# Kernel optimization log

Hardware: AMD Instinct MI355X
Metric: run time of the kernel (lower is better)

Reference implementation:

```python
import jax, jax.numpy as jnp
import numpy as np

K = 20
IN_CH = 128
OUT_CH = 128


def setup_inputs() -> dict:
    key = jax.random.key(0)
    k1, k2, k3, k4, k5, k6 = jax.random.split(key, 6)
    B, N = 2, 8192
    pos = jax.random.normal(k1, (B, N, 3), dtype=jnp.float32)
    features = jax.random.normal(k2, (B, N, IN_CH), dtype=jnp.float32)
    # fc = Linear(2C -> OUT) , ReLU, Linear(OUT -> OUT); stored as [in, out]
    s1 = 1.0 / np.sqrt(2 * IN_CH)
    s2 = 1.0 / np.sqrt(OUT_CH)
    W1 = jax.random.uniform(k3, (2 * IN_CH, OUT_CH), jnp.float32, -s1, s1)
    b1 = jax.random.uniform(k4, (OUT_CH,), jnp.float32, -s1, s1)
    W2 = jax.random.uniform(k5, (OUT_CH, OUT_CH), jnp.float32, -s2, s2)
    b2 = jax.random.uniform(k6, (OUT_CH,), jnp.float32, -s2, s2)
    return {"pos": pos, "features": features, "W1": W1, "b1": b1, "W2": W2, "b2": b2}


def reference(pos, features, W1, b1, W2, b2):
    B, N, _ = pos.shape
    C = features.shape[-1]
    p = pos.reshape(-1, 3)            # [BN, 3] (cross-batch, as in original)
    f = features.reshape(-1, C)       # [BN, C]
    # squared pairwise distances (same top-k ordering as torch.cdist)
    sq = jnp.sum(p * p, axis=-1)
    d2 = sq[:, None] + sq[None, :] - 2.0 * (p @ p.T)   # [BN, BN]
    _, knn_idx = jax.lax.top_k(-d2, K)                 # [BN, K] smallest dists
    nb = f[knn_idx]                                    # [BN, K, C] gather
    center = jnp.broadcast_to(f[:, None, :], nb.shape)
    edge = jnp.concatenate([center, nb - center], axis=-1)   # [BN, K, 2C]
    h = jax.nn.relu(jnp.einsum('nkc,cd->nkd', edge, W1) + b1)
    h = jnp.einsum('nkd,de->nke', h, W2) + b2          # [BN, K, OUT]
    x = jnp.max(h, axis=1)                             # max aggregation
    return x.reshape(B, N, -1)
```

## Files before the change

kernel.cpp:

```cpp
#include <hip/hip_runtime.h>

typedef unsigned short u16;
typedef unsigned int   u32;
typedef unsigned long long u64;
typedef short s16x8 __attribute__((ext_vector_type(8)));
typedef float f32x4 __attribute__((ext_vector_type(4)));

#define NPTS   16384
#define KNNK   20
#define SLOTS3 12
#define TRIG3  4
#define NSEG   16
#define PSZ    1024
#define SCAP   24

#define MFMA_BF16 __builtin_amdgcn_mfma_f32_16x16x32_bf16

__device__ __forceinline__ u16 f2bf(float x) {
  u32 u = __builtin_bit_cast(u32, x);
  u32 r = (u + 0x7FFFu + ((u >> 16) & 1u)) >> 16;
  return (u16)r;
}
__device__ __forceinline__ float bf2f(u16 b) {
  u32 u = ((u32)b) << 16;
  return __builtin_bit_cast(float, u);
}
__device__ __forceinline__ float dist2(float4 qp, float4 cd) {
  float dot = fmaf(qp.x, cd.x, fmaf(qp.y, cd.y, qp.z * cd.z));
  return fmaf(-2.0f, dot, qp.w + cd.w);
}

__global__ __launch_bounds__(256) void knnconv_prep(const float* __restrict__ pos,
                                                    float4* __restrict__ pos4) {
  int i = blockIdx.x * 256 + threadIdx.x;
  float x = pos[i * 3 + 0], y = pos[i * 3 + 1], z = pos[i * 3 + 2];
  float sq = (x * x + y * y) + z * z;
  pos4[i] = make_float4(x, y, z, sq);
}

__global__ __launch_bounds__(1024) void knnconv_s0(const float4* __restrict__ pos4,
                                                   float* __restrict__ tau) {
  __shared__ float sd[SLOTS3 * 1024];
  __shared__ float md[16][64][4];
  __shared__ float4 stg[16][2][64];
  const int tid  = threadIdx.x;
  const int lane = tid & 63;
  const int wv   = tid >> 6;
  const int qg   = blockIdx.x;
  const int q    = qg * 64 + lane;
  const float4 qp = pos4[q];
  const float INF = __builtin_inff();

  float t0v = INF, t1v = INF, t2v = INF;
  float thrF = INF;
  int cnt = 0;
  const int kbase = wv * 256;

#define FLUSH3()                                                      \
  { _Pragma("unroll 1")                                               \
    for (int e = 0; e < SLOTS3; e += 2) {                             \
      if (!__any(e < cnt)) break;                                     \
      float lo = (e     < cnt) ? sd[e * 1024 + tid]       : INF;      \
      float hi = (e + 1 < cnt) ? sd[(e + 1) * 1024 + tid] : INF;      \
      float a_ = fminf(lo, hi), b_ = fmaxf(lo, hi);                   \
      lo = a_; hi = b_;                                               \
      { float m = fminf(lo, t0v), x = fmaxf(lo, t0v);                 \
        t0v = m; lo = fminf(x, hi); hi = fmaxf(x, hi); }              \
      { float m = fminf(lo, t1v), x = fmaxf(lo, t1v);                 \
        t1v = m; lo = fminf(x, hi); hi = fmaxf(x, hi); }              \
      t2v = fminf(lo, t2v);                                           \
    }                                                                 \
    thrF = t2v;                                                       \
    cnt = 0; }

  float4 r = pos4[(kbase + 0 * 64 + lane) * 4];
  stg[wv][0][lane] = r;
  r = pos4[(kbase + 1 * 64 + lane) * 4];
  #pragma unroll 1
  for (int w = 0; w < 4; ++w) {
    const float4* wb = stg[wv][w & 1];
    #pragma unroll 1
    for (int g8 = 0; g8 < 64; g8 += 8) {
      #pragma unroll
      for (int u = 0; u < 8; ++u) {
        float d2 = dist2(qp, wb[g8 + u]);
        sd[cnt * 1024 + tid] = d2;
        cnt += (d2 < thrF) ? 1 : 0;
      }
      if (__any(cnt >= TRIG3)) { FLUSH3(); }
    }
    if (w < 3) {
      stg[wv][(w + 1) & 1][lane] = r;
      if (w < 2) r = pos4[(kbase + (w + 2) * 64 + lane) * 4];
    }
  }
  FLUSH3();

  md[wv][lane][0] = t0v;
  md[wv][lane][1] = t1v;
  md[wv][lane][2] = t2v;
  md[wv][lane][3] = INF;
  __syncthreads();

  if (tid < 64) {
    int ql = tid;
    int h0=0,h1=0,h2=0,h3=0,h4=0,h5=0,h6=0,h7=0;
    int h8=0,h9=0,h10=0,h11=0,h12=0,h13=0,h14=0,h15=0;
    float last = INF;
    for (int r2 = 0; r2 < KNNK; ++r2) {
      float c0 = md[ 0][ql][h0],  c1 = md[ 1][ql][h1];
      float c2 = md[ 2][ql][h2],  c3 = md[ 3][ql][h3];
      float c4 = md[ 4][ql][h4],  c5 = md[ 5][ql][h5];
      float c6 = md[ 6][ql][h6],  c7 = md[ 7][ql][h7];
      float c8 = md[ 8][ql][h8],  c9 = md[ 9][ql][h9];
      float cA = md[10][ql][h10], cB = md[11][ql][h11];
      float cC = md[12][ql][h12], cD = md[13][ql][h13];
      float cE = md[14][ql][h14], cF = md[15][ql][h15];
      float bv = c0; int bw = 0;
      if (c1 < bv) { bv = c1; bw = 1; }
      if (c2 < bv) { bv = c2; bw = 2; }
      if (c3 < bv) { bv = c3; bw = 3; }
      if (c4 < bv) { bv = c4; bw = 4; }
      if (c5 < bv) { bv = c5; bw = 5; }
      if (c6 < bv) { bv = c6; bw = 6; }
      if (c7 < bv) { bv = c7; bw = 7; }
      if (c8 < bv) { bv = c8; bw = 8; }
      if (c9 < bv) { bv = c9; bw = 9; }
      if (cA < bv) { bv = cA; bw = 10; }
      if (cB < bv) { bv = cB; bw = 11; }
      if (cC < bv) { bv = cC; bw = 12; }
      if (cD < bv) { bv = cD; bw = 13; }
      if (cE < bv) { bv = cE; bw = 14; }
      if (cF < bv) { bv = cF; bw = 15; }
      last = bv;
      h0  += (bw==0);  h1  += (bw==1);  h2  += (bw==2);  h3  += (bw==3);
      h4  += (bw==4);  h5  += (bw==5);  h6  += (bw==6);  h7  += (bw==7);
      h8  += (bw==8);  h9  += (bw==9);  h10 += (bw==10); h11 += (bw==11);
      h12 += (bw==12); h13 += (bw==13); h14 += (bw==14); h15 += (bw==15);
    }
    tau[qg * 64 + ql] = last * 1.00001f;
  }
}

__global__ __launch_bounds__(256) void knnconv_s1x(const float4* __restrict__ pos4,
                                                   const float* __restrict__ tau,
                                                   u16* __restrict__ g1,
                                                   u16* __restrict__ gcnt) {
  const int tid  = threadIdx.x;
  const int lane = tid & 63;
  const int wv   = __builtin_amdgcn_readfirstlane(tid >> 6);
  const int qg   = blockIdx.x >> 2;
  const int pb   = blockIdx.x & 3;
  const int part = pb * 4 + wv;
  const int q    = qg * 64 + lane;
  const float4 P = pos4[q];
  const float Qx = P.x, Qy = P.y, Qz = P.z;
  const float Qt = 0.5f * (tau[q] - P.w);
  const int cbase = part * PSZ;
  const float4* cp = pos4 + cbase;
  u16* seg = g1 + (q * NSEG + part) * SCAP;
  int cnt = 0;

  #pragma unroll 1
  for (int t0 = 0; t0 < PSZ; t0 += 16) {
    float4 c[16];
    #pragma unroll
    for (int u = 0; u < 16; ++u) c[u] = cp[t0 + u];
    #pragma unroll
    for (int u = 0; u < 16; ++u) {
      float dot = fmaf(Qx, c[u].x, fmaf(Qy, c[u].y, Qz * c[u].z));
      float lhs = fmaf(0.5f, c[u].w, -dot);
      if (lhs <= Qt) {
        if (cnt < SCAP) seg[cnt] = (u16)(cbase + t0 + u);
        ++cnt;
      }
    }
  }
  gcnt[q * NSEG + part] = (u16)min(cnt, SCAP);
}

__global__ __launch_bounds__(256) void knnconv_s2(const float4* __restrict__ pos4,
                                                  const u16* __restrict__ g1,
                                                  const u16* __restrict__ gcnt,
                                                  u16* __restrict__ knn_out) {
  __shared__ u64 keys[16 * 256];
  __shared__ int Tq[16];
  const int tid = threadIdx.x;
  const int iq = tid >> 4, s = tid & 15;
  const int q0 = blockIdx.x * 16;
  const int q = q0 + iq;

  #pragma unroll
  for (int i = 0; i < 16; ++i) keys[i * 256 + tid] = ~0ULL;
  __syncthreads();

  int off = 0, T = 0;
  #pragma unroll
  for (int j = 0; j < NSEG; ++j) {
    int cj = gcnt[q * NSEG + j];
    off += (j < s) ? cj : 0;
    T += cj;
  }
  if (s == 15) Tq[iq] = min(T, 256);
  int myc = gcnt[q * NSEG + s];
  float4 P = pos4[q];
  for (int i = 0; i < myc; ++i) {
    int pos = off + i;
    if (pos >= 256) break;
    int cidx = (int)g1[(q * NSEG + s) * SCAP + i];
    float4 C = pos4[cidx];
    double qx = P.x, qy = P.y, qz = P.z;
    double cx = C.x, cy = C.y, cz = C.z;
    double sqq = qx * qx + qy * qy + qz * qz;
    double sqc = cx * cx + cy * cy + cz * cz;
    double dot = qx * cx + qy * cy + qz * cz;
    double d   = (sqq + sqc) - 2.0 * dot;
    float df = fmaxf((float)d, 0.0f);
    keys[iq * 256 + pos] = ((u64)__builtin_bit_cast(u32, df) << 14) | (u32)cidx;
  }
  __syncthreads();

  #pragma unroll 1
  for (int t = 0; t < 16; ++t) {
    int T2 = Tq[t];
    if (tid < T2) {
      u64 kj = keys[t * 256 + tid];
      const u64* row = keys + t * 256;
      int r = 0;
      for (int k = 0; k < T2; ++k) r += (row[k] < kj) ? 1 : 0;
      if (r < KNNK)
        knn_out[(q0 + t) * KNNK + r] = (u16)(kj & 0x3FFFu);
    }
  }
}

__global__ __launch_bounds__(256) void knnconv_wprep(const float* __restrict__ W1,
                                                     const float* __restrict__ W2,
                                                     u16* __restrict__ w1bf,
                                                     u16* __restrict__ w2bf) {
  int b = blockIdx.x;
  if (b < 128) {
    int e = b * 256 + threadIdx.x;
    int n = e >> 7, kk = e & 127;
    float v;
    if (n < 128) v = W1[(128 + kk) * 128 + n];
    else { int n2 = n - 128; v = W1[kk * 128 + n2] - W1[(128 + kk) * 128 + n2]; }
    w1bf[(n * 256 + ((kk * 2) ^ ((n & 7) << 4))) >> 1] = f2bf(v);
  } else {
    int e = (b - 128) * 256 + threadIdx.x;
    int n = e >> 7, kk = e & 127;
    w2bf[(n * 256 + ((kk * 2) ^ ((n & 7) << 4))) >> 1] = f2bf(W2[kk * 128 + n]);
  }
}

__global__ __launch_bounds__(256) void knnconv_prec(const float* __restrict__ feat,
                                                    const u16* __restrict__ w1bf,
                                                    const float* __restrict__ b1,
                                                    u16* __restrict__ a_out,
                                                    float* __restrict__ c_out) {
  __shared__ char sW[65536];
  __shared__ char sF[16384];
  const int tid = threadIdx.x;
  {
    const uint4* src = (const uint4*)w1bf;
    uint4* dst = (uint4*)sW;
    #pragma unroll
    for (int r = 0; r < 16; ++r) dst[r * 256 + tid] = src[r * 256 + tid];
  }
  {
    int sub = tid & 15, r0 = tid >> 4;
    int m0 = blockIdx.x * 64;
    for (int rr = 0; rr < 4; ++rr) {
      int r = r0 + rr * 16;
      const float* src = feat + (m0 + r) * 128 + sub * 8;
      float4 v0 = *(const float4*)src;
      float4 v1 = *(const float4*)(src + 4);
      u32 p0 = (u32)f2bf(v0.x) | ((u32)f2bf(v0.y) << 16);
      u32 p1 = (u32)f2bf(v0.z) | ((u32)f2bf(v0.w) << 16);
      u32 p2 = (u32)f2bf(v1.x) | ((u32)f2bf(v1.y) << 16);
      u32 p3 = (u32)f2bf(v1.z) | ((u32)f2bf(v1.w) << 16);
      *(uint4*)(sF + r * 256 + ((sub * 16) ^ ((r & 7) << 4))) = make_uint4(p0, p1, p2, p3);
    }
  }
  __syncthreads();
  const int lane = tid & 63, wv = tid >> 6;
  const int l15 = lane & 15, l4 = lane >> 4;
  f32x4 acc[4][4];
  #pragma unroll
  for (int a = 0; a < 4; ++a)
    #pragma unroll
    for (int b = 0; b < 4; ++b) acc[a][b] = (f32x4){0.f, 0.f, 0.f, 0.f};
  #pragma unroll
  for (int kk = 0; kk < 4; ++kk) {
    int kb = kk * 64 + l4 * 16;
    s16x8 af[4], bfr[4];
    #pragma unroll
    for (int mt = 0; mt < 4; ++mt) {
      int row = mt * 16 + l15;
      af[mt] = *(const s16x8*)(sF + row * 256 + (kb ^ ((row & 7) << 4)));
    }
    #pragma unroll
    for (int nt = 0; nt < 4; ++nt) {
      int n = (wv * 4 + nt) * 16 + l15;
      bfr[nt] = *(const s16x8*)(sW + n * 256 + (kb ^ ((n & 7) << 4)));
    }
    #pragma unroll
    for (int mt = 0; mt < 4; ++mt)
      #pragma unroll
      for (int nt = 0; nt < 4; ++nt)
        acc[mt][nt] = MFMA_BF16(af[mt], bfr[nt], acc[mt][nt], 0, 0, 0);
  }
  int m0 = blockIdx.x * 64;
  #pragma unroll
  for (int nt = 0; nt < 4; ++nt) {
    int n = (wv * 4 + nt) * 16 + l15;
    float bias = (n >= 128) ? b1[n - 128] : 0.0f;
    #pragma unroll
    for (int mt = 0; mt < 4; ++mt)
      #pragma unroll
      for (int r = 0; r < 4; ++r) {
        int m = m0 + mt * 16 + l4 * 4 + r;
        float v = acc[mt][nt][r];
        if (n < 128) a_out[m * 128 + n] = f2bf(v);
        else         c_out[m * 128 + (n - 128)] = v + bias;
      }
  }
}

__global__ __launch_bounds__(256) void knnconv_conv(const u16* __restrict__ knn,
                                                    const u16* __restrict__ a_in,
                                                    const float* __restrict__ c_in,
                                                    const u16* __restrict__ w2bf,
                                                    const float* __restrict__ b2,
                                                    float* __restrict__ out) {
  __shared__ char lds[77824];
  char* sA = lds;
  char* sW = lds + 40960;
  char* sC = lds + 73728;
  const int tid = threadIdx.x;
  const int q0 = blockIdx.x * 8;

  {
    int row = tid >> 5, ch4 = (tid & 31) * 4;
    *(float4*)(sC + (row * 128 + ch4) * 4) = *(const float4*)(c_in + (q0 + row) * 128 + ch4);
  }
  __syncthreads();
  {
    const uint4* src = (const uint4*)w2bf;
    uint4* dst = (uint4*)sW;
    #pragma unroll
    for (int r = 0; r < 8; ++r) dst[r * 256 + tid] = src[r * 256 + tid];
  }
  {
    int sub = tid & 15, rr = tid >> 4;
    for (int p = 0; p < 10; ++p) {
      int r = p * 16 + rr;
      int il = r / 20;
      int ke = r - il * 20;
      int idx = (int)knn[(q0 + il) * KNNK + ke];
      uint4 av = *(const uint4*)(a_in + idx * 128 + sub * 8);
      float4 c0 = *(const float4*)(sC + (il * 128 + sub * 8) * 4);
      float4 c1 = *(const float4*)(sC + (il * 128 + sub * 8 + 4) * 4);
      float h0 = fmaxf(bf2f((u16)(av.x & 0xFFFF)) + c0.x, 0.f);
      float h1 = fmaxf(bf2f((u16)(av.x >> 16))    + c0.y, 0.f);
      float h2 = fmaxf(bf2f((u16)(av.y & 0xFFFF)) + c0.z, 0.f);
      float h3 = fmaxf(bf2f((u16)(av.y >> 16))    + c0.w, 0.f);
      float h4 = fmaxf(bf2f((u16)(av.z & 0xFFFF)) + c1.x, 0.f);
      float h5 = fmaxf(bf2f((u16)(av.z >> 16))    + c1.y, 0.f);
      float h6 = fmaxf(bf2f((u16)(av.w & 0xFFFF)) + c1.z, 0.f);
      float h7 = fmaxf(bf2f((u16)(av.w >> 16))    + c1.w, 0.f);
      u32 p0 = (u32)f2bf(h0) | ((u32)f2bf(h1) << 16);
      u32 p1 = (u32)f2bf(h2) | ((u32)f2bf(h3) << 16);
      u32 p2 = (u32)f2bf(h4) | ((u32)f2bf(h5) << 16);
      u32 p3 = (u32)f2bf(h6) | ((u32)f2bf(h7) << 16);
      *(uint4*)(sA + r * 256 + ((sub * 16) ^ ((r & 7) << 4))) = make_uint4(p0, p1, p2, p3);
    }
  }
  __syncthreads();
  const int lane = tid & 63, wv = tid >> 6;
  const int l15 = lane & 15, l4 = lane >> 4;
  f32x4 acc[10][2];
  #pragma unroll
  for (int mt = 0; mt < 10; ++mt) { acc[mt][0] = (f32x4){0,0,0,0}; acc[mt][1] = (f32x4){0,0,0,0}; }
  #pragma unroll
  for (int kk = 0; kk < 4; ++kk) {
    int kb = kk * 64 + l4 * 16;
    s16x8 b0, b1r;
    { int n = (wv * 2 + 0) * 16 + l15; b0  = *(const s16x8*)(sW + n * 256 + (kb ^ ((n & 7) << 4))); }
    { int n = (wv * 2 + 1) * 16 + l15; b1r = *(const s16x8*)(sW + n * 256 + (kb ^ ((n & 7) << 4))); }
    #pragma unroll
    for (int mt = 0; mt < 10; ++mt) {
      int row = mt * 16 + l15;
      s16x8 a = *(const s16x8*)(sA + row * 256 + (kb ^ ((row & 7) << 4)));
      acc[mt][0] = MFMA_BF16(a, b0,  acc[mt][0], 0, 0, 0);
      acc[mt][1] = MFMA_BF16(a, b1r, acc[mt][1], 0, 0, 0);
    }
  }
  __syncthreads();
  #pragma unroll
  for (int mt = 0; mt < 10; ++mt)
    #pragma unroll
    for (int nt = 0; nt < 2; ++nt) {
      int n = (wv * 2 + nt) * 16 + l15;
      #pragma unroll
      for (int r = 0; r < 4; ++r) {
        int row = mt * 16 + l4 * 4 + r;
        *(u16*)(sA + row * 256 + n * 2) = f2bf(acc[mt][nt][r]);
      }
    }
  __syncthreads();
  {
    int ch = tid & 127, g = tid >> 7;
    float bias = b2[ch];
    for (int pp = 0; pp < 4; ++pp) {
      int qq = pp * 2 + g;
      float mx = -__builtin_inff();
      #pragma unroll
      for (int e = 0; e < KNNK; ++e)
        mx = fmaxf(mx, bf2f(*(const u16*)(sA + (qq * 20 + e) * 256 + ch * 2)));
      out[(q0 + qq) * 128 + ch] = mx + bias;
    }
  }
}

extern "C" void kernel_launch(void* const* d_in, const int* in_sizes, int n_in,
                              void* d_out, int out_size, void* d_ws, size_t ws_size,
                              hipStream_t stream) {
  const float* pos  = (const float*)d_in[0];
  const float* feat = (const float*)d_in[1];
  const float* W1   = (const float*)d_in[2];
  const float* b1   = (const float*)d_in[3];
  const float* W2   = (const float*)d_in[4];
  const float* b2   = (const float*)d_in[5];
  float* out = (float*)d_out;
  char* ws = (char*)d_ws;
  float4* pos4  = (float4*)ws;
  u16*    w1bf  = (u16*)ws;
  u16*    w2bf  = (u16*)(ws + 65536);
  u16*    knn   = (u16*)(ws + 262144);
  u16*    g1    = (u16*)(ws + 917504);
  u16*    a_buf = (u16*)(ws + 917504);
  float*  c_buf = (float*)(ws + 5111808);
  u16*    gcnt  = (u16*)(ws + 13500416);
  float*  tau   = (float*)(ws + 14024704);
  if (ws_size < 14090240) return;

  knnconv_prep<<<64, 256, 0, stream>>>(pos, pos4);
  knnconv_s0<<<256, 1024, 0, stream>>>(pos4, tau);
  knnconv_s1x<<<1024, 256, 0, stream>>>(pos4, tau, g1, gcnt);
  knnconv_s2<<<1024, 256, 0, stream>>>(pos4, g1, gcnt, knn);
  knnconv_wprep<<<192, 256, 0, stream>>>(W1, W2, w1bf, w2bf);
  knnconv_prec<<<256, 256, 0, stream>>>(feat, w1bf, b1, a_buf, c_buf);
  knnconv_conv<<<2048, 256, 0, stream>>>(knn, a_buf, c_buf, w2bf, b2, out);
}
```

Baseline: 207.1 us.

## Keep W2 fragments in registers and pre-reduce max per lane before LDS

The conv kernel no longer stages W2 in shared memory; each wave loads its B fragments for W2 straight from global memory into registers once. The epilogue reduces each lane's four accumulator rows to a single max and writes it in fp32 to a padded LDS buffer. Each output is then the max of five group values, replacing the per-element bf16 scatter and the 20-way reduction. Together these shrink LDS from about 76KB to 44KB, which can allow more blocks per CU. The cost is extra registers and a small change in numerics, since the max is now taken in fp32 rather than after bf16 rounding.

Measured after the change: 196.1 us. -5.3%, faster.

```diff
diff --git a/kernel.cpp b/kernel.cpp
--- a/kernel.cpp
+++ b/kernel.cpp
@@ -333,24 +333,30 @@
                                                     const u16* __restrict__ w2bf,
                                                     const float* __restrict__ b2,
                                                     float* __restrict__ out) {
-  __shared__ char lds[77824];
+  __shared__ char lds[45056];
   char* sA = lds;
-  char* sW = lds + 40960;
-  char* sC = lds + 73728;
+  float* sG = (float*)lds;
+  char* sC = lds + 40960;
   const int tid = threadIdx.x;
   const int q0 = blockIdx.x * 8;
+  const int lane = tid & 63, wv = tid >> 6;
+  const int l15 = lane & 15, l4 = lane >> 4;
+
+  s16x8 bfr[4][2];
+  #pragma unroll
+  for (int kk = 0; kk < 4; ++kk)
+    #pragma unroll
+    for (int nt = 0; nt < 2; ++nt) {
+      int n = (wv * 2 + nt) * 16 + l15;
+      int kb = kk * 64 + l4 * 16;
+      bfr[kk][nt] = *(const s16x8*)((const char*)w2bf + n * 256 + (kb ^ ((n & 7) << 4)));
+    }
 
   {
     int row = tid >> 5, ch4 = (tid & 31) * 4;
     *(float4*)(sC + (row * 128 + ch4) * 4) = *(const float4*)(c_in + (q0 + row) * 128 + ch4);
   }
   __syncthreads();
-  {
-    const uint4* src = (const uint4*)w2bf;
-    uint4* dst = (uint4*)sW;
-    #pragma unroll
-    for (int r = 0; r < 8; ++r) dst[r * 256 + tid] = src[r * 256 + tid];
-  }
   {
     int sub = tid & 15, rr = tid >> 4;
     for (int p = 0; p < 10; ++p) {
@@ -377,48 +383,45 @@
     }
   }
   __syncthreads();
-  const int lane = tid & 63, wv = tid >> 6;
-  const int l15 = lane & 15, l4 = lane >> 4;
   f32x4 acc[10][2];
   #pragma unroll
   for (int mt = 0; mt < 10; ++mt) { acc[mt][0] = (f32x4){0,0,0,0}; acc[mt][1] = (f32x4){0,0,0,0}; }
   #pragma unroll
   for (int kk = 0; kk < 4; ++kk) {
     int kb = kk * 64 + l4 * 16;
-    s16x8 b0, b1r;
-    { int n = (wv * 2 + 0) * 16 + l15; b0  = *(const s16x8*)(sW + n * 256 + (kb ^ ((n & 7) << 4))); }
-    { int n = (wv * 2 + 1) * 16 + l15; b1r = *(const s16x8*)(sW + n * 256 + (kb ^ ((n & 7) << 4))); }
     #pragma unroll
     for (int mt = 0; mt < 10; ++mt) {
       int row = mt * 16 + l15;
       s16x8 a = *(const s16x8*)(sA + row * 256 + (kb ^ ((row & 7) << 4)));
-      acc[mt][0] = MFMA_BF16(a, b0,  acc[mt][0], 0, 0, 0);
-      acc[mt][1] = MFMA_BF16(a, b1r, acc[mt][1], 0, 0, 0);
-    }
-  }
-  __syncthreads();
-  #pragma unroll
-  for (int mt = 0; mt < 10; ++mt)
+      acc[mt][0] = MFMA_BF16(a, bfr[kk][0], acc[mt][0], 0, 0, 0);
+      acc[mt][1] = MFMA_BF16(a, bfr[kk][1], acc[mt][1], 0, 0, 0);
+    }
+  }
+  __syncthreads();
+  #pragma unroll
+  for (int mt = 0; mt < 10; ++mt) {
+    int g = mt * 4 + l4;
     #pragma unroll
     for (int nt = 0; nt < 2; ++nt) {
-      int n = (wv * 2 + nt) * 16 + l15;
-      #pragma unroll
-      for (int r = 0; r < 4; ++r) {
-        int row = mt * 16 + l4 * 4 + r;
-        *(u16*)(sA + row * 256 + n * 2) = f2bf(acc[mt][nt][r]);
-      }
-    }
+      int col = (wv * 2 + nt) * 16 + l15;
+      f32x4 a4 = acc[mt][nt];
+      float gm = fmaxf(fmaxf(a4[0], a4[1]), fmaxf(a4[2], a4[3]));
+      sG[g * 129 + col] = gm;
+    }
+  }
   __syncthreads();
   {
-    int ch = tid & 127, g = tid >> 7;
-    float bias = b2[ch];
-    for (int pp = 0; pp < 4; ++pp) {
-      int qq = pp * 2 + g;
-      float mx = -__builtin_inff();
-      #pragma unroll
-      for (int e = 0; e < KNNK; ++e)
-        mx = fmaxf(mx, bf2f(*(const u16*)(sA + (qq * 20 + e) * 256 + ch * 2)));
-      out[(q0 + qq) * 128 + ch] = mx + bias;
+    #pragma unroll
+    for (int e = 0; e < 4; ++e) {
+      int elem = e * 256 + tid;
+      int qq = elem >> 7, ch = elem & 127;
+      const float* gp = sG + (qq * 5) * 129 + ch;
+      float mx = gp[0];
+      mx = fmaxf(mx, gp[129]);
+      mx = fmaxf(mx, gp[258]);
+      mx = fmaxf(mx, gp[387]);
+      mx = fmaxf(mx, gp[516]);
+      out[(q0 + qq) * 128 + ch] = mx + b2[ch];
     }
   }
 }
```
